# Kernel optimization log

Hardware: AMD Instinct MI355X
Metric: run time of the kernel (lower is better)

Reference implementation:

```python
import jax, jax.numpy as jnp
import numpy as np

N_NODES = 500_000
N_FEAT = 16
HIDDEN = 32
N_EDGES = 8_000_000


def setup_inputs() -> dict:
    key = jax.random.key(0)
    ks = jax.random.split(key, 12)
    x = jax.random.normal(ks[0], (N_NODES, N_FEAT), dtype=jnp.float32)
    edge_index = jax.random.randint(ks[1], (2, N_EDGES), 0, N_NODES, dtype=jnp.int32)
    edge_weight = jax.random.uniform(ks[2], (N_EDGES,), dtype=jnp.float32)
    h = 0.1 * jax.random.normal(ks[3], (N_NODES, HIDDEN), dtype=jnp.float32)
    c = 0.1 * jax.random.normal(ks[4], (N_NODES, HIDDEN), dtype=jnp.float32)
    s = 0.1  # glorot-ish scale
    # Gate order along axis 0: (i, f, c~, o). K=1 ChebConv == Linear.
    W_x = s * jax.random.normal(ks[5], (4, N_FEAT, HIDDEN), dtype=jnp.float32)
    b_x = s * jax.random.normal(ks[6], (4, HIDDEN), dtype=jnp.float32)
    W_h = s * jax.random.normal(ks[7], (4, HIDDEN, HIDDEN), dtype=jnp.float32)
    b_h = s * jax.random.normal(ks[8], (4, HIDDEN), dtype=jnp.float32)
    w_c = s * jax.random.normal(ks[9], (3, HIDDEN), dtype=jnp.float32)  # peephole (i, f, o)
    b_g = s * jax.random.normal(ks[10], (4, HIDDEN), dtype=jnp.float32)  # per-gate bias b_i,b_f,b_c,b_o
    W_lin = s * jax.random.normal(ks[11], (HIDDEN, 1), dtype=jnp.float32)
    b_lin = jnp.zeros((1,), dtype=jnp.float32)
    return {"x": x, "edge_index": edge_index, "edge_weight": edge_weight,
            "h": h, "c": c, "W_x": W_x, "b_x": b_x, "W_h": W_h, "b_h": b_h,
            "w_c": w_c, "b_g": b_g, "W_lin": W_lin, "b_lin": b_lin}


def reference(x, edge_index, edge_weight, h, c, W_x, b_x, W_h, b_h, w_c, b_g, W_lin, b_lin):
    # GConvLSTM with K=1: each ChebConv degenerates to a single linear map
    # (Tx_0 = x, out = x @ W_0 + b); edge_index / edge_weight are unused by the math.
    # gx, gh: [4, N, H] — stacked (i, f, c~, o) gate pre-activations.
    gx = jnp.einsum('nf,gfh->gnh', x, W_x) + b_x[:, None, :]
    gh = jnp.einsum('nh,gho->gno', h, W_h) + b_h[:, None, :]
    s = gx + gh
    i = jax.nn.sigmoid(s[0] + w_c[0] * c + b_g[0])
    f = jax.nn.sigmoid(s[1] + w_c[1] * c + b_g[1])
    t = jnp.tanh(s[2] + b_g[2])
    c_new = f * c + i * t
    o = jax.nn.sigmoid(s[3] + w_c[2] * c_new + b_g[3])
    h0 = o * jnp.tanh(c_new)
    out = jax.nn.relu(h0) @ W_lin + b_lin  # [N, 1]
    return (out, h0, c_new)
```

## Files before the change

### kernel.cpp

```cpp
#include <hip/hip_runtime.h>
#include <hip/hip_bf16.h>

#define NF 16
#define NH 32
#define LOG2E  1.44269504088896340736f
#define TILE_NODES 32

#define T_WORDS 2560
#define XW 0
#define HW 512
#define CW 1536
#define HOUT 0
#define COUT 1152

typedef short bf16x8 __attribute__((ext_vector_type(8)));
typedef float f32x16 __attribute__((ext_vector_type(16)));

#if __has_builtin(__builtin_amdgcn_exp2f)
#define EXP2(x) __builtin_amdgcn_exp2f(x)
#else
#define EXP2(x) exp2f(x)
#endif

__device__ __forceinline__ short f2bf(float f) {
    __hip_bfloat16 b = __float2bfloat16(f);
    return *reinterpret_cast<short*>(&b);
}

__device__ __forceinline__ bf16x8 cvt8(float4 a, float4 b) {
    bf16x8 r;
    r[0] = f2bf(a.x); r[1] = f2bf(a.y); r[2] = f2bf(a.z); r[3] = f2bf(a.w);
    r[4] = f2bf(b.x); r[5] = f2bf(b.y); r[6] = f2bf(b.z); r[7] = f2bf(b.w);
    return r;
}

__device__ __forceinline__ float sig2(float v) {
    return __builtin_amdgcn_rcpf(1.0f + EXP2(-v));
}
__device__ __forceinline__ float tanh2(float v) {
    return 1.0f - 2.0f * __builtin_amdgcn_rcpf(1.0f + EXP2(v));
}

__device__ __forceinline__ void gload_lds16(const float* g, float* l) {
    __builtin_amdgcn_global_load_lds(
        (const __attribute__((address_space(1))) void*)g,
        (__attribute__((address_space(3))) void*)l, 16, 0, 0);
}

struct Frags { bf16x8 w[4][4]; bf16x8 a3; };

__global__ void prep_kernel(const float* __restrict__ Wx, const float* __restrict__ Wh,
                            const float* __restrict__ bx, const float* __restrict__ bh,
                            const float* __restrict__ bg, const float* __restrict__ wc,
                            short* __restrict__ Wpack, float* __restrict__ wcs)
{
    int t = blockIdx.x * blockDim.x + threadIdx.x;
    if (t < 4 * 4 * 64) {
        int g  = t >> 8;
        int ks = (t >> 6) & 3;
        int l  = t & 63;
        int col  = l & 31;
        int half = l >> 5;
        float scale = (g == 2) ? 2.0f * LOG2E : LOG2E;
        #pragma unroll
        for (int e = 0; e < 8; ++e) {
            int gk = ks * 16 + half * 8 + e;
            float w;
            if (gk < NF)            w = Wx[(g * NF + gk) * NH + col];
            else if (gk < NF + NH)  w = Wh[(g * NH + (gk - NF)) * NH + col];
            else if (gk == 48)      w = bx[g * NH + col] + bh[g * NH + col] + bg[g * NH + col];
            else                    w = 0.0f;
            Wpack[t * 8 + e] = f2bf(w * scale);
        }
    }
    if (t < 3 * NH) wcs[t] = wc[t] * LOG2E;
}

__device__ __forceinline__ void prefetch_tile(const float* __restrict__ x,
                                              const float* __restrict__ hin,
                                              const float* __restrict__ cin,
                                              long nb, float* ws, int lane)
{
    asm volatile("" ::: "memory");
    const float* xb = x   + nb * NF;
    const float* hb = hin + nb * NH;
    const float* cb = cin + nb * NH;
    #pragma unroll
    for (int i = 0; i < 2; ++i) {
        int u = i * 64 + lane;
        int src = (u & ~3) | ((u & 3) ^ ((u >> 2) & 3));
        gload_lds16(xb + src * 4, ws + XW + i * 256);
    }
    #pragma unroll
    for (int i = 0; i < 4; ++i) {
        int u = i * 64 + lane;
        int src = (u & ~7) | ((u & 7) ^ ((u >> 3) & 7));
        gload_lds16(hb + src * 4, ws + HW + i * 256);
    }
    #pragma unroll
    for (int i = 0; i < 4; ++i) {
        int u = i * 64 + lane;
        int src = (u & ~7) | ((u & 7) ^ ((u >> 3) & 7));
        gload_lds16(cb + src * 4, ws + CW + i * 256);
    }
    asm volatile("" ::: "memory");
}

__device__ __forceinline__ void do_tile(float* ws, long nb, const Frags& F,
                                        const float* __restrict__ wcs,
                                        const float* __restrict__ Wlin, float bl,
                                        float* __restrict__ out,
                                        float* __restrict__ h0o,
                                        float* __restrict__ co, int lane)
{
    const int col  = lane & 31;
    const int half = lane >> 5;
    const int c3 = col & 3, c7 = col & 7;

    asm volatile("s_waitcnt vmcnt(10)" ::: "memory");

    float4 x0 = *(const float4*)&ws[XW + (col * 4 + ((2 * half)     ^ c3)) * 4];
    float4 x1 = *(const float4*)&ws[XW + (col * 4 + ((2 * half + 1) ^ c3)) * 4];
    float4 h0 = *(const float4*)&ws[HW + (col * 8 + ((2 * half)     ^ c7)) * 4];
    float4 h1 = *(const float4*)&ws[HW + (col * 8 + ((2 * half + 1) ^ c7)) * 4];
    float4 h2 = *(const float4*)&ws[HW + (col * 8 + ((4 + 2 * half) ^ c7)) * 4];
    float4 h3 = *(const float4*)&ws[HW + (col * 8 + ((5 + 2 * half) ^ c7)) * 4];
    bf16x8 a0 = cvt8(x0, x1), a1 = cvt8(h0, h1), a2 = cvt8(h2, h3);

    float4 cv4[4];
    #pragma unroll
    for (int jg = 0; jg < 4; ++jg)
        cv4[jg] = *(const float4*)&ws[CW + (col * 8 + ((2 * jg + half) ^ c7)) * 4];

    f32x16 acc[4];
    #pragma unroll
    for (int g = 0; g < 4; ++g) {
        #pragma unroll
        for (int r = 0; r < 16; ++r) acc[g][r] = 0.0f;
        acc[g] = __builtin_amdgcn_mfma_f32_32x32x16_bf16(F.w[g][0], a0,   acc[g], 0, 0, 0);
        acc[g] = __builtin_amdgcn_mfma_f32_32x32x16_bf16(F.w[g][1], a1,   acc[g], 0, 0, 0);
        acc[g] = __builtin_amdgcn_mfma_f32_32x32x16_bf16(F.w[g][2], a2,   acc[g], 0, 0, 0);
        acc[g] = __builtin_amdgcn_mfma_f32_32x32x16_bf16(F.w[g][3], F.a3, acc[g], 0, 0, 0);
    }

    float outacc = 0.0f;
    const float c2l = 2.0f * LOG2E;
    #pragma unroll
    for (int jg = 0; jg < 4; ++jg) {
        const int jbase = jg * 8 + 4 * half;
        const float4 w0 = *(const float4*)(wcs + 0 * NH + jbase);
        const float4 w1 = *(const float4*)(wcs + 1 * NH + jbase);
        const float4 w2 = *(const float4*)(wcs + 2 * NH + jbase);
        const float4 wl = *(const float4*)(Wlin + jbase);
        float h4[4], c4[4];
        #pragma unroll
        for (int q = 0; q < 4; ++q) {
            const int r = jg * 4 + q;
            const float ci = ((const float*)&cv4[jg])[q];
            const float ig = sig2(fmaf(((const float*)&w0)[q], ci, acc[0][r]));
            const float fg = sig2(fmaf(((const float*)&w1)[q], ci, acc[1][r]));
            const float tg = tanh2(acc[2][r]);
            const float cn = fg * ci + ig * tg;
            const float og = sig2(fmaf(((const float*)&w2)[q], cn, acc[3][r]));
            const float hh = og * tanh2(cn * c2l);
            c4[q] = cn;
            h4[q] = hh;
            outacc = fmaf(fmaxf(hh, 0.0f), ((const float*)&wl)[q], outacc);
        }
        *(float4*)&ws[HOUT + col * 36 + jbase] = make_float4(h4[0], h4[1], h4[2], h4[3]);
        *(float4*)&ws[COUT + col * 36 + jbase] = make_float4(c4[0], c4[1], c4[2], c4[3]);
    }

    float* hrow = h0o + nb * NH;
    float* crow = co  + nb * NH;
    #pragma unroll
    for (int rep = 0; rep < 4; ++rep) {
        const int tt = lane + rep * 64;
        const int nd = tt >> 3, j4 = (tt & 7) * 4;
        float4 vh = *(const float4*)&ws[HOUT + nd * 36 + j4];
        float4 vc = *(const float4*)&ws[COUT + nd * 36 + j4];
        *(float4*)(hrow + tt * 4) = vh;
        *(float4*)(crow + tt * 4) = vc;
    }

    outacc += __shfl_xor(outacc, 32, 64);
    if (half == 0) out[nb + col] = outacc + bl;
}

__global__ __launch_bounds__(256, 2) void lstm_pipe_kernel(
    const float* __restrict__ x, const float* __restrict__ hin,
    const float* __restrict__ cin,
    const float* __restrict__ Wlin, const float* __restrict__ blin,
    const short* __restrict__ Wpack, const float* __restrict__ wcs,
    float* __restrict__ out, float* __restrict__ h0o, float* __restrict__ co,
    int ntiles, int wstride)
{
    __shared__ float bufA[4][T_WORDS];
    __shared__ float bufB[4][T_WORDS];

    const int lane = threadIdx.x & 63;
    const int wave = threadIdx.x >> 6;
    float* wsA = bufA[wave];
    float* wsB = bufB[wave];

    Frags F;
    #pragma unroll
    for (int g = 0; g < 4; ++g)
        #pragma unroll
        for (int ks = 0; ks < 4; ++ks)
            F.w[g][ks] = *(const bf16x8*)(Wpack + (((g * 4) + ks) * 64 + lane) * 8);
    #pragma unroll
    for (int e = 0; e < 8; ++e) F.a3[e] = 0;
    if ((lane >> 5) == 0) F.a3[0] = (short)0x3F80;
    const float bl = blin[0];

    int t = blockIdx.x * 4 + wave;
    if (t >= ntiles) return;
    prefetch_tile(x, hin, cin, (long)t * TILE_NODES, wsA, lane);

    for (;;) {
        int t1 = t + wstride;
        if (t1 < ntiles) prefetch_tile(x, hin, cin, (long)t1 * TILE_NODES, wsB, lane);
        do_tile(wsA, (long)t * TILE_NODES, F, wcs, Wlin, bl, out, h0o, co, lane);
        if (t1 >= ntiles) break;

        int t2 = t1 + wstride;
        if (t2 < ntiles) prefetch_tile(x, hin, cin, (long)t2 * TILE_NODES, wsA, lane);
        do_tile(wsB, (long)t1 * TILE_NODES, F, wcs, Wlin, bl, out, h0o, co, lane);
        if (t2 >= ntiles) break;
        t = t2;
    }
}

extern "C" void kernel_launch(void* const* d_in, const int* in_sizes, int n_in,
                              void* d_out, int out_size, void* d_ws, size_t ws_size,
                              hipStream_t stream) {
    const float* x    = (const float*)d_in[0];
    const float* h    = (const float*)d_in[3];
    const float* c    = (const float*)d_in[4];
    const float* Wx   = (const float*)d_in[5];
    const float* bx   = (const float*)d_in[6];
    const float* Wh   = (const float*)d_in[7];
    const float* bh   = (const float*)d_in[8];
    const float* wc   = (const float*)d_in[9];
    const float* bg   = (const float*)d_in[10];
    const float* Wlin = (const float*)d_in[11];
    const float* blin = (const float*)d_in[12];

    const int N = in_sizes[0] / NF;
    const int ntiles = N / TILE_NODES;

    float* out = (float*)d_out;
    float* h0o = out + N;
    float* co  = h0o + (size_t)N * NH;

    short* Wpack = (short*)d_ws;
    float* wcs   = (float*)((char*)d_ws + 4 * 4 * 64 * 8 * sizeof(short));

    prep_kernel<<<4, 256, 0, stream>>>(Wx, Wh, bx, bh, bg, wc, Wpack, wcs);

    const int grid = 512;
    const int wstride = grid * 4;
    lstm_pipe_kernel<<<grid, 256, 0, stream>>>(
        x, h, c, Wlin, blin, Wpack, wcs, out, h0o, co, ntiles, wstride);
}
```

Measured before the change: 65.88 us.

## Deepen LDS prefetch pipeline, hoist swizzle offsets, use nontemporal stores

Restructures the per-wave loop so two tiles are always in flight. The next-next tile's prefetch is issued right after the current tile is computed, and waits use vmcnt counts that also account for the store instructions. Swizzled source offsets are computed once per thread instead of per prefetch, and h/c/out writes use nontemporal stores to avoid polluting cache. Tail prefetches clamp to the last tile instead of branching, which adds redundant loads. The hand-tuned vmcnt values risk races if the instruction counts differ from what is assumed.

```diff
diff --git a/kernel.cpp b/kernel.cpp
--- a/kernel.cpp
+++ b/kernel.cpp
@@ -15,6 +15,7 @@
 
 typedef short bf16x8 __attribute__((ext_vector_type(8)));
 typedef float f32x16 __attribute__((ext_vector_type(16)));
+typedef float f32x4  __attribute__((ext_vector_type(4)));
 
 #if __has_builtin(__builtin_amdgcn_exp2f)
 #define EXP2(x) __builtin_amdgcn_exp2f(x)
@@ -45,6 +46,11 @@
     __builtin_amdgcn_global_load_lds(
         (const __attribute__((address_space(1))) void*)g,
         (__attribute__((address_space(3))) void*)l, 16, 0, 0);
+}
+
+__device__ __forceinline__ void nt_store4(float* p, float4 v) {
+    f32x4 w = { v.x, v.y, v.z, v.w };
+    __builtin_nontemporal_store(w, (f32x4*)p);
 }
 
 struct Frags { bf16x8 w[4][4]; bf16x8 a3; };
@@ -79,30 +85,19 @@
 __device__ __forceinline__ void prefetch_tile(const float* __restrict__ x,
                                               const float* __restrict__ hin,
                                               const float* __restrict__ cin,
-                                              long nb, float* ws, int lane)
+                                              long nb, float* ws,
+                                              const int* xoff, const int* hoff)
 {
     asm volatile("" ::: "memory");
     const float* xb = x   + nb * NF;
     const float* hb = hin + nb * NH;
     const float* cb = cin + nb * NH;
     #pragma unroll
-    for (int i = 0; i < 2; ++i) {
-        int u = i * 64 + lane;
-        int src = (u & ~3) | ((u & 3) ^ ((u >> 2) & 3));
-        gload_lds16(xb + src * 4, ws + XW + i * 256);
-    }
-    #pragma unroll
-    for (int i = 0; i < 4; ++i) {
-        int u = i * 64 + lane;
-        int src = (u & ~7) | ((u & 7) ^ ((u >> 3) & 7));
-        gload_lds16(hb + src * 4, ws + HW + i * 256);
-    }
-    #pragma unroll
-    for (int i = 0; i < 4; ++i) {
-        int u = i * 64 + lane;
-        int src = (u & ~7) | ((u & 7) ^ ((u >> 3) & 7));
-        gload_lds16(cb + src * 4, ws + CW + i * 256);
-    }
+    for (int i = 0; i < 2; ++i) gload_lds16(xb + xoff[i], ws + XW + i * 256);
+    #pragma unroll
+    for (int i = 0; i < 4; ++i) gload_lds16(hb + hoff[i], ws + HW + i * 256);
+    #pragma unroll
+    for (int i = 0; i < 4; ++i) gload_lds16(cb + hoff[i], ws + CW + i * 256);
     asm volatile("" ::: "memory");
 }
 
@@ -116,8 +111,6 @@
     const int col  = lane & 31;
     const int half = lane >> 5;
     const int c3 = col & 3, c7 = col & 7;
-
-    asm volatile("s_waitcnt vmcnt(10)" ::: "memory");
 
     float4 x0 = *(const float4*)&ws[XW + (col * 4 + ((2 * half)     ^ c3)) * 4];
     float4 x1 = *(const float4*)&ws[XW + (col * 4 + ((2 * half + 1) ^ c3)) * 4];
@@ -179,12 +172,12 @@
         const int nd = tt >> 3, j4 = (tt & 7) * 4;
         float4 vh = *(const float4*)&ws[HOUT + nd * 36 + j4];
         float4 vc = *(const float4*)&ws[COUT + nd * 36 + j4];
-        *(float4*)(hrow + tt * 4) = vh;
-        *(float4*)(crow + tt * 4) = vc;
+        nt_store4(hrow + tt * 4, vh);
+        nt_store4(crow + tt * 4, vc);
     }
 
     outacc += __shfl_xor(outacc, 32, 64);
-    if (half == 0) out[nb + col] = outacc + bl;
+    if (half == 0) __builtin_nontemporal_store(outacc + bl, &out[nb + col]);
 }
 
 __global__ __launch_bounds__(256, 2) void lstm_pipe_kernel(
@@ -200,8 +193,8 @@
 
     const int lane = threadIdx.x & 63;
     const int wave = threadIdx.x >> 6;
-    float* wsA = bufA[wave];
-    float* wsB = bufB[wave];
+    float* cur = bufA[wave];
+    float* oth = bufB[wave];
 
     Frags F;
     #pragma unroll
@@ -214,21 +207,41 @@
     if ((lane >> 5) == 0) F.a3[0] = (short)0x3F80;
     const float bl = blin[0];
 
+    int xoff[2], hoff[4];
+    #pragma unroll
+    for (int i = 0; i < 2; ++i) {
+        int u = i * 64 + lane;
+        xoff[i] = ((u & ~3) | ((u & 3) ^ ((u >> 2) & 3))) * 4;
+    }
+    #pragma unroll
+    for (int i = 0; i < 4; ++i) {
+        int u = i * 64 + lane;
+        hoff[i] = ((u & ~7) | ((u & 7) ^ ((u >> 3) & 7))) * 4;
+    }
+
+    const int S = wstride;
+    const int last = ntiles - 1;
     int t = blockIdx.x * 4 + wave;
-    if (t >= ntiles) return;
-    prefetch_tile(x, hin, cin, (long)t * TILE_NODES, wsA, lane);
-
+
+    prefetch_tile(x, hin, cin, (long)t * TILE_NODES, cur, xoff, hoff);
+    {
+        int t1 = t + S; if (t1 > last) t1 = last;
+        prefetch_tile(x, hin, cin, (long)t1 * TILE_NODES, oth, xoff, hoff);
+    }
+
+    bool first = true;
     for (;;) {
-        int t1 = t + wstride;
-        if (t1 < ntiles) prefetch_tile(x, hin, cin, (long)t1 * TILE_NODES, wsB, lane);
-        do_tile(wsA, (long)t * TILE_NODES, F, wcs, Wlin, bl, out, h0o, co, lane);
-        if (t1 >= ntiles) break;
-
-        int t2 = t1 + wstride;
-        if (t2 < ntiles) prefetch_tile(x, hin, cin, (long)t2 * TILE_NODES, wsA, lane);
-        do_tile(wsB, (long)t1 * TILE_NODES, F, wcs, Wlin, bl, out, h0o, co, lane);
-        if (t2 >= ntiles) break;
-        t = t2;
+        if (first) { asm volatile("s_waitcnt vmcnt(10)" ::: "memory"); first = false; }
+        else       { asm volatile("s_waitcnt vmcnt(19)" ::: "memory"); }
+
+        do_tile(cur, (long)t * TILE_NODES, F, wcs, Wlin, bl, out, h0o, co, lane);
+
+        int tn = t + 2 * S; if (tn > last) tn = last;
+        prefetch_tile(x, hin, cin, (long)tn * TILE_NODES, cur, xoff, hoff);
+
+        t += S;
+        if (t >= ntiles) break;
+        float* tmp = cur; cur = oth; oth = tmp;
     }
 }
 
```

New measurement: 58.18 us. -11.7%, faster.
